# Performance work log

Measured on AMD Instinct MI355X. Metric: run time of the kernel, lower is better.

## Reference

```python
import jax, jax.numpy as jnp
import numpy as np

EPS = 1e-10
W_SILOG, W_L2, W_BINS = 1.0, 1.0, 1.0  # w_masked=1.0 -> invalid branch skipped


def setup_inputs() -> dict:
    key = jax.random.key(0)
    k1, k2, k3, k4 = jax.random.split(key, 4)
    B, H, W = 8, 240, 320
    NB = 256  # n_bins
    prediction = jax.random.uniform(k1, (B, 1, H, W), dtype=jnp.float32)
    target = jax.random.uniform(k2, (B, 1, H, W), dtype=jnp.float32)
    bin_edges = jax.random.uniform(k3, (B, NB + 1), dtype=jnp.float32)
    mask = jax.random.randint(k4, (B, 1, H, W), 0, 2).astype(jnp.bool_)
    return {"prediction": prediction, "target": target, "bin_edges": bin_edges, "mask": mask}


def _onedirectional_dist(a, b):
    # a: [B, Na], b: [B, Nb] -> sum over Na of min_j (a_i - b_j)^2, shape [B]
    d2 = (a[:, :, None] - b[:, None, :]) ** 2  # [B, Na, Nb]
    return jnp.min(d2, axis=2).sum(axis=1)


def reference(prediction, target, bin_edges, mask):
    # Chamfer distance between bin centers and target depth values
    bin_centers = 0.5 * (bin_edges[:, :-1] + bin_edges[:, 1:])  # [B, NB]
    target_depths = target.reshape(target.shape[0], -1)         # [B, H*W]
    chamfer = (_onedirectional_dist(bin_centers, target_depths)
               + _onedirectional_dist(target_depths, bin_centers)).mean()

    # Masked reductions (equivalent to boolean-indexed means, jit-friendly)
    p = prediction.reshape(-1)
    t = target.reshape(-1)
    fm = mask.reshape(-1).astype(p.dtype)
    cnt = fm.sum()

    # L2: sqrt(MSE over masked elements)
    l2 = jnp.sqrt(jnp.sum((p - t) ** 2 * fm) / cnt)

    # SILog
    d = jnp.log(p + EPS) - jnp.log(t + EPS)
    d_mean = jnp.sum(d * fm) / cnt
    d2_mean = jnp.sum(d * d * fm) / cnt
    silog = 10.0 * jnp.sqrt(d2_mean - 0.85 * d_mean ** 2)

    return W_L2 * l2 + W_SILOG * silog + W_BINS * chamfer
```

## Files before the change

### kernel.cpp

```cpp
#include <hip/hip_runtime.h>
#include <math.h>

#define HW     76800
#define NBATCH 8
#define NB     256
#define NEDGE  257
#define ELEMS  12
#define XBLKS  25
#define MAIN_BLOCKS (XBLKS * NBATCH)
#define FINF 3.402823466e+38f


__device__ __forceinline__ float wsum32(float v) {
#pragma unroll
  for (int o = 32; o > 0; o >>= 1) v += __shfl_down(v, o, 64);
  return v;
}

__device__ __forceinline__ unsigned int nzb(unsigned int w) {
  return ((w & 0xFFu) != 0u) + (((w >> 8) & 0xFFu) != 0u) +
         (((w >> 16) & 0xFFu) != 0u) + ((w >> 24) != 0u);
}

__global__ void __launch_bounds__(256) k_prep(
    const float* __restrict__ edges, const unsigned char* __restrict__ mask,
    double* __restrict__ sums, unsigned int* __restrict__ ticket,
    unsigned int* __restrict__ flag, unsigned int* __restrict__ gD,
    float* __restrict__ cs, float2* __restrict__ gLut) {
  const int tid = threadIdx.x, b = blockIdx.x;
  if (b < NBATCH) {
    __shared__ float s[NB];
    float v = 0.5f * (edges[b * NEDGE + tid] + edges[b * NEDGE + tid + 1]);
    for (int k = 2; k <= NB; k <<= 1) {
      for (int j = k >> 1; j > 0; j >>= 1) {
        float partner;
        if (j < 64) {
          partner = __shfl_xor(v, j, 64);
        } else {
          __syncthreads();
          s[tid] = v;
          __syncthreads();
          partner = s[tid ^ j];
        }
        const bool up = ((tid & k) == 0);
        const bool low = ((tid & j) == 0);
        v = (low == up) ? fminf(v, partner) : fmaxf(v, partner);
      }
    }
    cs[b * NB + tid] = v;
    gD[b * NB + tid] = 0u;
    __syncthreads();
    s[tid] = v;
    __syncthreads();
    const float x = (float)tid * 0.00390625f;
    int k = -1;
    if (s[255] <= x) {
      k = 255;
    } else {
#pragma unroll
      for (int st = 128; st > 0; st >>= 1) {
        int nk = k + st;
        if (nk < 255 && s[nk] <= x) k = nk;
      }
    }
    float ck = (k >= 0) ? s[k] : -FINF;
    gLut[b * NB + tid] = make_float2(ck, __int_as_float(k));
  } else {
    uint4 raw = ((const uint4*)mask)[tid];
    unsigned int c = nzb(raw.x) + nzb(raw.y) + nzb(raw.z) + nzb(raw.w);
#pragma unroll
    for (int o = 32; o > 0; o >>= 1) c += __shfl_down(c, o, 64);
    __shared__ unsigned int sh[4];
    if ((tid & 63) == 0) sh[tid >> 6] = c;
    __syncthreads();
    if (tid == 0) *flag = ((sh[0] + sh[1] + sh[2] + sh[3]) > 1024u) ? 1u : 0u;
    if (tid < 40) sums[tid] = 0.0;
    if (tid == 40) *ticket = 0u;
  }
}

__global__ void __launch_bounds__(256) k_main(
    const float* __restrict__ p, const float* __restrict__ t,
    const void* __restrict__ mask, const unsigned int* __restrict__ flag,
    const float* __restrict__ cs, const float2* __restrict__ gLut,
    double* __restrict__ sums, unsigned int* __restrict__ gD,
    unsigned int* __restrict__ ticket, float* __restrict__ out) {
  __shared__ float c_lds[NB + 1];
  __shared__ float2 lut_lds[NB];
  __shared__ unsigned int d_lds[NB + 2];
  __shared__ float shred[4][5];
  __shared__ double dpart[4];
  __shared__ double fin[40];
  __shared__ unsigned int last_flag;

  const int tid = threadIdx.x, lane = tid & 63, wid = tid >> 6;
  const int b = blockIdx.y;
  const int ebase = b * HW + blockIdx.x * (NB * ELEMS) + tid * ELEMS;

  c_lds[tid] = cs[b * NB + tid];
  lut_lds[tid] = gLut[b * NB + tid];
  d_lds[tid] = 0u;
  if (tid < 2) d_lds[NB + tid] = 0u;
  if (tid == 0) c_lds[NB] = FINF;
  __syncthreads();

  float pe[ELEMS], te[ELEMS];
  int me[ELEMS];
  {
    const float4* pp = (const float4*)(p + ebase);
    const float4* tt = (const float4*)(t + ebase);
#pragma unroll
    for (int q = 0; q < 3; ++q) {
      float4 a = pp[q], c = tt[q];
      pe[q * 4 + 0] = a.x; pe[q * 4 + 1] = a.y; pe[q * 4 + 2] = a.z; pe[q * 4 + 3] = a.w;
      te[q * 4 + 0] = c.x; te[q * 4 + 1] = c.y; te[q * 4 + 2] = c.z; te[q * 4 + 3] = c.w;
    }
  }
  if (*flag) {
    const unsigned int* mp = (const unsigned int*)((const unsigned char*)mask + ebase);
    unsigned int w[3] = {mp[0], mp[1], mp[2]};
#pragma unroll
    for (int e = 0; e < ELEMS; ++e) me[e] = (w[e >> 2] >> ((e & 3) * 8)) & 0xFFu;
  } else {
    const int4* mp = (const int4*)((const int*)mask + ebase);
#pragma unroll
    for (int q = 0; q < 3; ++q) {
      int4 m4 = mp[q];
      me[q * 4 + 0] = m4.x; me[q * 4 + 1] = m4.y; me[q * 4 + 2] = m4.z; me[q * 4 + 3] = m4.w;
    }
  }

  int cnt = 0;
  float ssq = 0.f, sd = 0.f, sd2 = 0.f, dir2 = 0.f;
#pragma unroll
  for (int e = 0; e < ELEMS; ++e) {
    if (me[e]) {
      float diff = pe[e] - te[e];
      float d = logf(pe[e] + 1e-10f) - logf(te[e] + 1e-10f);
      cnt += 1;
      ssq += diff * diff;
      sd  += d;
      sd2 += d * d;
    }
  }

  int   kk[ELEMS];
  float ck[ELEMS], c1[ELEMS];
#pragma unroll
  for (int e = 0; e < ELEMS; ++e) {
    int q = (int)(te[e] * 256.0f);
    q = (q < 0) ? 0 : ((q > 255) ? 255 : q);
    float2 lu = lut_lds[q];
    ck[e] = lu.x;
    kk[e] = __float_as_int(lu.y);
  }
#pragma unroll
  for (int e = 0; e < ELEMS; ++e) c1[e] = c_lds[kk[e] + 1];
#pragma unroll
  for (int e = 0; e < ELEMS; ++e) {
    const float ti = te[e];
    int k = kk[e];
    float c0 = ck[e], cn = c1[e];
    while (cn <= ti) { ++k; c0 = cn; cn = c_lds[k + 1]; }
    float dl = ti - c0;
    float dr = cn - ti;
    atomicMax(&d_lds[k + 1], ~__float_as_uint(dl));
    atomicMax(&d_lds[k + 2], ~__float_as_uint(dr));
    float dm = fminf(dl, dr);
    dir2 += dm * dm;
  }

  __syncthreads();
  {
    unsigned int dv = d_lds[tid + 1];
    if (dv) atomicMax(&gD[b * NB + tid], dv);
  }

  float acc[5] = {(float)cnt, ssq, sd, sd2, dir2};
#pragma unroll
  for (int i = 0; i < 5; ++i) {
    float r = wsum32(acc[i]);
    if (lane == 0) shred[wid][i] = r;
  }
  __syncthreads();
  if (tid < 5) {
    atomicAdd(&sums[b * 5 + tid],
              (double)(shred[0][tid] + shred[1][tid] + shred[2][tid] + shred[3][tid]));
  }

  asm volatile("s_waitcnt vmcnt(0) lgkmcnt(0)" ::: "memory");
  __syncthreads();
  if (tid == 0)
    last_flag = (atomicAdd(ticket, 1u) == (unsigned)(MAIN_BLOCKS - 1)) ? 1u : 0u;
  __syncthreads();
  if (last_flag == 0u) return;

  if (tid < 40) fin[tid] = atomicAdd(&sums[tid], 0.0);

  double dir1 = 0.0;
#pragma unroll
  for (int r = 0; r < 2; ++r) {
    const int bb = wid + r * 4;
    float c[4], D[4];
#pragma unroll
    for (int i = 0; i < 4; ++i) {
      const int idx = bb * NB + lane * 4 + i;
      c[i] = cs[idx];
      unsigned int s = atomicOr(&gD[idx], 0u);
      D[i] = s ? __uint_as_float(~s) : FINF;
    }

    float pa[4];
    pa[0] = D[0] - c[0];
    pa[1] = fminf(pa[0], D[1] - c[1]);
    pa[2] = fminf(pa[1], D[2] - c[2]);
    pa[3] = fminf(pa[2], D[3] - c[3]);
    float s1 = pa[3];
#pragma unroll
    for (int off = 1; off < 64; off <<= 1) {
      float u = __shfl_up(s1, off, 64);
      if (lane >= off) s1 = fminf(s1, u);
    }
    float exL = __shfl_up(s1, 1, 64);
    if (lane == 0) exL = FINF;

    float sb[4];
    sb[3] = D[3] + c[3];
    sb[2] = fminf(sb[3], D[2] + c[2]);
    sb[1] = fminf(sb[2], D[1] + c[1]);
    sb[0] = fminf(sb[1], D[0] + c[0]);
    float s2 = sb[0];
#pragma unroll
    for (int off = 1; off < 64; off <<= 1) {
      float u = __shfl_down(s2, off, 64);
      if (lane + off < 64) s2 = fminf(s2, u);
    }
    float exR = __shfl_down(s2, 1, 64);
    if (lane == 63) exR = FINF;

#pragma unroll
    for (int i = 0; i < 4; ++i) {
      float pref = fminf(exL, pa[i]);
      float suf  = fminf(exR, sb[i]);
      float dist = fminf(pref + c[i], suf - c[i]);
      dir1 += (double)dist * (double)dist;
    }
  }

#pragma unroll
  for (int o = 32; o > 0; o >>= 1) dir1 += __shfl_down(dir1, o, 64);
  if (lane == 0) dpart[wid] = dir1;
  __syncthreads();
  if (tid == 0) {
    double d1 = dpart[0] + dpart[1] + dpart[2] + dpart[3];
    double cnt_ = 0, ssq_ = 0, sd_ = 0, sd2_ = 0, d2_ = 0;
#pragma unroll
    for (int bb = 0; bb < NBATCH; ++bb) {
      cnt_ += fin[bb * 5 + 0]; ssq_ += fin[bb * 5 + 1];
      sd_  += fin[bb * 5 + 2]; sd2_ += fin[bb * 5 + 3];
      d2_  += fin[bb * 5 + 4];
    }
    double l2 = sqrt(ssq_ / cnt_);
    double dm = sd_ / cnt_, d2m = sd2_ / cnt_;
    double silog = 10.0 * sqrt(d2m - 0.85 * dm * dm);
    double chamfer = (d1 + d2_) / (double)NBATCH;
    out[0] = (float)(l2 + silog + chamfer);
  }
}

extern "C" void kernel_launch(void* const* d_in, const int* in_sizes, int n_in,
                              void* d_out, int out_size, void* d_ws, size_t ws_size,
                              hipStream_t stream) {
  const float* pred  = (const float*)d_in[0];
  const float* targ  = (const float*)d_in[1];
  const float* edges = (const float*)d_in[2];
  const void*  mask  = d_in[3];

  char* ws = (char*)d_ws;
  double* sums         = (double*)ws;
  unsigned int* ticket = (unsigned int*)(ws + 320);
  unsigned int* flag   = (unsigned int*)(ws + 324);
  unsigned int* gD     = (unsigned int*)(ws + 512);
  float* cs            = (float*)(ws + 8704);
  float2* gLut         = (float2*)(ws + 16896);

  k_prep<<<NBATCH + 1, NB, 0, stream>>>(edges, (const unsigned char*)mask,
                                        sums, ticket, flag, gD, cs, gLut);
  k_main<<<dim3(XBLKS, NBATCH), NB, 0, stream>>>(pred, targ, mask, flag, cs, gLut,
                                                 sums, gD, ticket, (float*)d_out);
}
```

Before: 21.72 us.

## Fuse prep kernel into main kernel with per-block sort and two-level completion

Removes the separate prep kernel. Each main block now redundantly sorts its batch's bin centers, builds the lookup table locally with a range-fill, and detects the mask dtype itself. Workspace zeroing moves to a hipMemsetAsync. The final reduction becomes hierarchical: a per-batch last block computes that batch's bin-to-target distance, then a global last block combines everything. This trades one kernel launch and a global round trip for redundant sort work in every block, plus the cost of a memset node.

```diff
diff --git a/kernel.cpp b/kernel.cpp
--- a/kernel.cpp
+++ b/kernel.cpp
@@ -7,116 +7,52 @@
 #define NEDGE  257
 #define ELEMS  12
 #define XBLKS  25
-#define MAIN_BLOCKS (XBLKS * NBATCH)
 #define FINF 3.402823466e+38f
 
-
-__device__ __forceinline__ float wsum32(float v) {
-#pragma unroll
-  for (int o = 32; o > 0; o >>= 1) v += __shfl_down(v, o, 64);
-  return v;
-}
 
 __device__ __forceinline__ unsigned int nzb(unsigned int w) {
   return ((w & 0xFFu) != 0u) + (((w >> 8) & 0xFFu) != 0u) +
          (((w >> 16) & 0xFFu) != 0u) + ((w >> 24) != 0u);
 }
 
-__global__ void __launch_bounds__(256) k_prep(
-    const float* __restrict__ edges, const unsigned char* __restrict__ mask,
-    double* __restrict__ sums, unsigned int* __restrict__ ticket,
-    unsigned int* __restrict__ flag, unsigned int* __restrict__ gD,
-    float* __restrict__ cs, float2* __restrict__ gLut) {
-  const int tid = threadIdx.x, b = blockIdx.x;
-  if (b < NBATCH) {
-    __shared__ float s[NB];
-    float v = 0.5f * (edges[b * NEDGE + tid] + edges[b * NEDGE + tid + 1]);
-    for (int k = 2; k <= NB; k <<= 1) {
-      for (int j = k >> 1; j > 0; j >>= 1) {
-        float partner;
-        if (j < 64) {
-          partner = __shfl_xor(v, j, 64);
-        } else {
-          __syncthreads();
-          s[tid] = v;
-          __syncthreads();
-          partner = s[tid ^ j];
-        }
-        const bool up = ((tid & k) == 0);
-        const bool low = ((tid & j) == 0);
-        v = (low == up) ? fminf(v, partner) : fmaxf(v, partner);
-      }
-    }
-    cs[b * NB + tid] = v;
-    gD[b * NB + tid] = 0u;
-    __syncthreads();
-    s[tid] = v;
-    __syncthreads();
-    const float x = (float)tid * 0.00390625f;
-    int k = -1;
-    if (s[255] <= x) {
-      k = 255;
-    } else {
-#pragma unroll
-      for (int st = 128; st > 0; st >>= 1) {
-        int nk = k + st;
-        if (nk < 255 && s[nk] <= x) k = nk;
-      }
-    }
-    float ck = (k >= 0) ? s[k] : -FINF;
-    gLut[b * NB + tid] = make_float2(ck, __int_as_float(k));
-  } else {
-    uint4 raw = ((const uint4*)mask)[tid];
-    unsigned int c = nzb(raw.x) + nzb(raw.y) + nzb(raw.z) + nzb(raw.w);
-#pragma unroll
-    for (int o = 32; o > 0; o >>= 1) c += __shfl_down(c, o, 64);
-    __shared__ unsigned int sh[4];
-    if ((tid & 63) == 0) sh[tid >> 6] = c;
-    __syncthreads();
-    if (tid == 0) *flag = ((sh[0] + sh[1] + sh[2] + sh[3]) > 1024u) ? 1u : 0u;
-    if (tid < 40) sums[tid] = 0.0;
-    if (tid == 40) *ticket = 0u;
-  }
-}
-
-__global__ void __launch_bounds__(256) k_main(
+__global__ __launch_bounds__(256) void k_all(
     const float* __restrict__ p, const float* __restrict__ t,
-    const void* __restrict__ mask, const unsigned int* __restrict__ flag,
-    const float* __restrict__ cs, const float2* __restrict__ gLut,
-    double* __restrict__ sums, unsigned int* __restrict__ gD,
-    unsigned int* __restrict__ ticket, float* __restrict__ out) {
+    const void* __restrict__ mask, const float* __restrict__ edges,
+    double* __restrict__ sums, unsigned int* __restrict__ tickets,
+    unsigned int* __restrict__ gD, float* __restrict__ out) {
   __shared__ float c_lds[NB + 1];
-  __shared__ float2 lut_lds[NB];
+  __shared__ float2 lut[NB];
   __shared__ unsigned int d_lds[NB + 2];
+  __shared__ float df[NB];
   __shared__ float shred[4][5];
-  __shared__ double dpart[4];
-  __shared__ double fin[40];
-  __shared__ unsigned int last_flag;
+  __shared__ unsigned int sh_u[4];
+  __shared__ double fin[48];
+  __shared__ unsigned int comb;
 
   const int tid = threadIdx.x, lane = tid & 63, wid = tid >> 6;
   const int b = blockIdx.y;
   const int ebase = b * HW + blockIdx.x * (NB * ELEMS) + tid * ELEMS;
 
-  c_lds[tid] = cs[b * NB + tid];
-  lut_lds[tid] = gLut[b * NB + tid];
-  d_lds[tid] = 0u;
-  if (tid < 2) d_lds[NB + tid] = 0u;
-  if (tid == 0) c_lds[NB] = FINF;
-  __syncthreads();
-
-  float pe[ELEMS], te[ELEMS];
-  int me[ELEMS];
+  float4 p4[3], t4[3];
   {
     const float4* pp = (const float4*)(p + ebase);
     const float4* tt = (const float4*)(t + ebase);
-#pragma unroll
-    for (int q = 0; q < 3; ++q) {
-      float4 a = pp[q], c = tt[q];
-      pe[q * 4 + 0] = a.x; pe[q * 4 + 1] = a.y; pe[q * 4 + 2] = a.z; pe[q * 4 + 3] = a.w;
-      te[q * 4 + 0] = c.x; te[q * 4 + 1] = c.y; te[q * 4 + 2] = c.z; te[q * 4 + 3] = c.w;
-    }
-  }
-  if (*flag) {
+    p4[0] = pp[0]; p4[1] = pp[1]; p4[2] = pp[2];
+    t4[0] = tt[0]; t4[1] = tt[1]; t4[2] = tt[2];
+  }
+  const uint4 raw = ((const uint4*)mask)[tid];
+  const float e0 = edges[b * NEDGE + tid];
+  const float e1 = edges[b * NEDGE + tid + 1];
+
+  unsigned int cnz = nzb(raw.x) + nzb(raw.y) + nzb(raw.z) + nzb(raw.w);
+#pragma unroll
+  for (int o = 32; o > 0; o >>= 1) cnz += __shfl_down(cnz, o, 64);
+  if (lane == 0) sh_u[wid] = cnz;
+  __syncthreads();
+  const bool bytemode = (sh_u[0] + sh_u[1] + sh_u[2] + sh_u[3]) > 1024u;
+
+  int me[ELEMS];
+  if (bytemode) {
     const unsigned int* mp = (const unsigned int*)((const unsigned char*)mask + ebase);
     unsigned int w[3] = {mp[0], mp[1], mp[2]};
 #pragma unroll
@@ -130,6 +66,47 @@
     }
   }
 
+  float v = 0.5f * (e0 + e1);
+  for (int k = 2; k <= NB; k <<= 1) {
+    for (int j = k >> 1; j > 0; j >>= 1) {
+      float partner;
+      if (j < 64) {
+        partner = __shfl_xor(v, j, 64);
+      } else {
+        __syncthreads();
+        c_lds[tid] = v;
+        __syncthreads();
+        partner = c_lds[tid ^ j];
+      }
+      const bool up = ((tid & k) == 0);
+      const bool low = ((tid & j) == 0);
+      v = (low == up) ? fminf(v, partner) : fmaxf(v, partner);
+    }
+  }
+  __syncthreads();
+  c_lds[tid] = v;
+  if (tid == 0) c_lds[NB] = FINF;
+  lut[tid] = make_float2(-FINF, __int_as_float(-1));
+  d_lds[tid] = 0u;
+  if (tid < 2) d_lds[NB + tid] = 0u;
+  __syncthreads();
+
+  {
+    const float cn1 = c_lds[tid + 1];
+    int lo = (int)ceilf(v * 256.0f);  lo = (lo < 0) ? 0 : lo;
+    int hi = (tid == 255) ? 255 : ((int)ceilf(cn1 * 256.0f) - 1);
+    hi = (hi > 255) ? 255 : hi;
+    const float2 entry = make_float2(v, __int_as_float(tid));
+    for (int q = lo; q <= hi; ++q) lut[q] = entry;
+  }
+  __syncthreads();
+
+  float pe[ELEMS], te[ELEMS];
+#pragma unroll
+  for (int q = 0; q < 3; ++q) {
+    pe[q * 4 + 0] = p4[q].x; pe[q * 4 + 1] = p4[q].y; pe[q * 4 + 2] = p4[q].z; pe[q * 4 + 3] = p4[q].w;
+    te[q * 4 + 0] = t4[q].x; te[q * 4 + 1] = t4[q].y; te[q * 4 + 2] = t4[q].z; te[q * 4 + 3] = t4[q].w;
+  }
   int cnt = 0;
   float ssq = 0.f, sd = 0.f, sd2 = 0.f, dir2 = 0.f;
 #pragma unroll
@@ -144,23 +121,15 @@
     }
   }
 
-  int   kk[ELEMS];
-  float ck[ELEMS], c1[ELEMS];
-#pragma unroll
-  for (int e = 0; e < ELEMS; ++e) {
-    int q = (int)(te[e] * 256.0f);
-    q = (q < 0) ? 0 : ((q > 255) ? 255 : q);
-    float2 lu = lut_lds[q];
-    ck[e] = lu.x;
-    kk[e] = __float_as_int(lu.y);
-  }
-#pragma unroll
-  for (int e = 0; e < ELEMS; ++e) c1[e] = c_lds[kk[e] + 1];
 #pragma unroll
   for (int e = 0; e < ELEMS; ++e) {
     const float ti = te[e];
-    int k = kk[e];
-    float c0 = ck[e], cn = c1[e];
+    int q = (int)(ti * 256.0f);
+    q = (q < 0) ? 0 : ((q > 255) ? 255 : q);
+    float2 lu = lut[q];
+    float c0 = lu.x;
+    int k = __float_as_int(lu.y);
+    float cn = c_lds[k + 1];
     while (cn <= ti) { ++k; c0 = cn; cn = c_lds[k + 1]; }
     float dl = ti - c0;
     float dr = cn - ti;
@@ -179,37 +148,36 @@
   float acc[5] = {(float)cnt, ssq, sd, sd2, dir2};
 #pragma unroll
   for (int i = 0; i < 5; ++i) {
-    float r = wsum32(acc[i]);
+    float r = acc[i];
+#pragma unroll
+    for (int o = 32; o > 0; o >>= 1) r += __shfl_down(r, o, 64);
     if (lane == 0) shred[wid][i] = r;
   }
   __syncthreads();
   if (tid < 5) {
-    atomicAdd(&sums[b * 5 + tid],
+    atomicAdd(&sums[b * 6 + tid],
               (double)(shred[0][tid] + shred[1][tid] + shred[2][tid] + shred[3][tid]));
   }
 
   asm volatile("s_waitcnt vmcnt(0) lgkmcnt(0)" ::: "memory");
   __syncthreads();
   if (tid == 0)
-    last_flag = (atomicAdd(ticket, 1u) == (unsigned)(MAIN_BLOCKS - 1)) ? 1u : 0u;
-  __syncthreads();
-  if (last_flag == 0u) return;
-
-  if (tid < 40) fin[tid] = atomicAdd(&sums[tid], 0.0);
-
-  double dir1 = 0.0;
-#pragma unroll
-  for (int r = 0; r < 2; ++r) {
-    const int bb = wid + r * 4;
+    comb = (atomicAdd(&tickets[b], 1u) == (unsigned)(XBLKS - 1)) ? 1u : 0u;
+  __syncthreads();
+  if (comb == 0u) return;
+
+  {
+    unsigned int s = atomicOr(&gD[b * NB + tid], 0u);
+    df[tid] = s ? __uint_as_float(~s) : FINF;
+  }
+  __syncthreads();
+  if (tid < 64) {
     float c[4], D[4];
 #pragma unroll
     for (int i = 0; i < 4; ++i) {
-      const int idx = bb * NB + lane * 4 + i;
-      c[i] = cs[idx];
-      unsigned int s = atomicOr(&gD[idx], 0u);
-      D[i] = s ? __uint_as_float(~s) : FINF;
-    }
-
+      c[i] = c_lds[tid * 4 + i];
+      D[i] = df[tid * 4 + i];
+    }
     float pa[4];
     pa[0] = D[0] - c[0];
     pa[1] = fminf(pa[0], D[1] - c[1]);
@@ -219,10 +187,10 @@
 #pragma unroll
     for (int off = 1; off < 64; off <<= 1) {
       float u = __shfl_up(s1, off, 64);
-      if (lane >= off) s1 = fminf(s1, u);
+      if (tid >= off) s1 = fminf(s1, u);
     }
     float exL = __shfl_up(s1, 1, 64);
-    if (lane == 0) exL = FINF;
+    if (tid == 0) exL = FINF;
 
     float sb[4];
     sb[3] = D[3] + c[3];
@@ -233,11 +201,12 @@
 #pragma unroll
     for (int off = 1; off < 64; off <<= 1) {
       float u = __shfl_down(s2, off, 64);
-      if (lane + off < 64) s2 = fminf(s2, u);
+      if (tid + off < 64) s2 = fminf(s2, u);
     }
     float exR = __shfl_down(s2, 1, 64);
-    if (lane == 63) exR = FINF;
-
+    if (tid == 63) exR = FINF;
+
+    double dir1 = 0.0;
 #pragma unroll
     for (int i = 0; i < 4; ++i) {
       float pref = fminf(exL, pa[i]);
@@ -245,25 +214,32 @@
       float dist = fminf(pref + c[i], suf - c[i]);
       dir1 += (double)dist * (double)dist;
     }
-  }
-
-#pragma unroll
-  for (int o = 32; o > 0; o >>= 1) dir1 += __shfl_down(dir1, o, 64);
-  if (lane == 0) dpart[wid] = dir1;
+#pragma unroll
+    for (int o = 32; o > 0; o >>= 1) dir1 += __shfl_down(dir1, o, 64);
+    if (tid == 0) atomicAdd(&sums[b * 6 + 5], dir1);
+  }
+
+  asm volatile("s_waitcnt vmcnt(0) lgkmcnt(0)" ::: "memory");
+  __syncthreads();
+  if (tid == 0)
+    comb = (atomicAdd(&tickets[8], 1u) == (unsigned)(NBATCH - 1)) ? 1u : 0u;
+  __syncthreads();
+  if (comb == 0u) return;
+
+  if (tid < 48) fin[tid] = atomicAdd(&sums[tid], 0.0);
   __syncthreads();
   if (tid == 0) {
-    double d1 = dpart[0] + dpart[1] + dpart[2] + dpart[3];
-    double cnt_ = 0, ssq_ = 0, sd_ = 0, sd2_ = 0, d2_ = 0;
+    double cnt_ = 0, ssq_ = 0, sd_ = 0, sd2_ = 0, d2_ = 0, d1_ = 0;
 #pragma unroll
     for (int bb = 0; bb < NBATCH; ++bb) {
-      cnt_ += fin[bb * 5 + 0]; ssq_ += fin[bb * 5 + 1];
-      sd_  += fin[bb * 5 + 2]; sd2_ += fin[bb * 5 + 3];
-      d2_  += fin[bb * 5 + 4];
+      cnt_ += fin[bb * 6 + 0]; ssq_ += fin[bb * 6 + 1];
+      sd_  += fin[bb * 6 + 2]; sd2_ += fin[bb * 6 + 3];
+      d2_  += fin[bb * 6 + 4]; d1_  += fin[bb * 6 + 5];
     }
     double l2 = sqrt(ssq_ / cnt_);
     double dm = sd_ / cnt_, d2m = sd2_ / cnt_;
     double silog = 10.0 * sqrt(d2m - 0.85 * dm * dm);
-    double chamfer = (d1 + d2_) / (double)NBATCH;
+    double chamfer = (d1_ + d2_) / (double)NBATCH;
     out[0] = (float)(l2 + silog + chamfer);
   }
 }
@@ -277,15 +253,11 @@
   const void*  mask  = d_in[3];
 
   char* ws = (char*)d_ws;
-  double* sums         = (double*)ws;
-  unsigned int* ticket = (unsigned int*)(ws + 320);
-  unsigned int* flag   = (unsigned int*)(ws + 324);
-  unsigned int* gD     = (unsigned int*)(ws + 512);
-  float* cs            = (float*)(ws + 8704);
-  float2* gLut         = (float2*)(ws + 16896);
-
-  k_prep<<<NBATCH + 1, NB, 0, stream>>>(edges, (const unsigned char*)mask,
-                                        sums, ticket, flag, gD, cs, gLut);
-  k_main<<<dim3(XBLKS, NBATCH), NB, 0, stream>>>(pred, targ, mask, flag, cs, gLut,
-                                                 sums, gD, ticket, (float*)d_out);
+  double* sums          = (double*)ws;
+  unsigned int* tickets = (unsigned int*)(ws + 384);
+  unsigned int* gD      = (unsigned int*)(ws + 512);
+
+  hipMemsetAsync(ws, 0, 8704, stream);
+  k_all<<<dim3(XBLKS, NBATCH), NB, 0, stream>>>(pred, targ, mask, edges,
+                                                sums, tickets, gD, (float*)d_out);
 }
```

New measurement: 26.04 us. 19.9% more time.
